# Performance work log

Measured on AMD Instinct MI355X. Metric: run time of the kernel, lower is better.

The kernel has to match this reference:

```python
import jax, jax.numpy as jnp
import numpy as np
from jax.scipy.special import logsumexp

BN_EPS = 1e-5
K_CLUSTERS = 32


def _conv1x1(x, W, b):
    # x: [B, Cin, N], W: [Cout, Cin] -> [B, Cout, N]
    return jnp.einsum('oc,bcn->bon', W, x) + b[None, :, None]


def _bn3(x, g, b):
    # BatchNorm1d (training mode, batch stats) over [B, C, N]
    m = x.mean(axis=(0, 2), keepdims=True)
    v = x.var(axis=(0, 2), keepdims=True)
    return g[None, :, None] * (x - m) / jnp.sqrt(v + BN_EPS) + b[None, :, None]


def _bn2(x, g, b):
    # BatchNorm1d (training mode, batch stats) over [B, C]
    m = x.mean(axis=0)
    v = x.var(axis=0)
    return g * (x - m) / jnp.sqrt(v + BN_EPS) + b


def _conv_proj(x, w1, b1, g1, t1, w2, b2, g2, t2, w3, b3):
    h = jax.nn.relu(_bn3(_conv1x1(x, w1, b1), g1, t1))
    h = jax.nn.relu(_bn3(_conv1x1(h, w2, b2), g2, t2))
    return _conv1x1(h, w3, b3)


def _mlp_proj(x, w1, b1, g1, t1, w2, b2, g2, t2, w3, b3):
    h = jax.nn.relu(_bn2(x @ w1.T + b1, g1, t1))
    h = jax.nn.relu(_bn2(h @ w2.T + b2, g2, t2))
    return h @ w3.T + b3


def _normalize(x, axis):
    n = jnp.linalg.norm(x, axis=axis, keepdims=True)
    return x / jnp.maximum(n, 1e-12)


def _sinkhorn_gamma(cost, p, q, eps=1e-3, thresh=1e-3, max_iter=25):
    # log-domain Sinkhorn with early stopping, mirrors the torch loop exactly
    logp = jnp.log(p + 1e-8)
    logq = jnp.log(q + 1e-8)

    def Kf(u, v):
        return (-cost + u[..., :, None] + v[..., None, :]) / eps

    def body(st):
        i, u, v, _ = st
        u0, v0 = u, v
        u = eps * (logp - logsumexp(Kf(u, v), axis=-1)) + u
        v = eps * (logq - logsumexp(Kf(u, v), axis=-2)) + v
        d = jnp.mean(jnp.sum(jnp.abs(u - u0), -1) + jnp.sum(jnp.abs(v - v0), -1))
        return i + 1, u, v, d

    def cond(st):
        return (st[0] < max_iter) & (st[3] >= thresh)

    init = (0, jnp.zeros_like(p), jnp.zeros_like(q), jnp.asarray(jnp.inf, cost.dtype))
    _, u, v, _ = jax.lax.while_loop(cond, body, init)
    return jnp.exp(Kf(u, v))


def _forward(features,
             cw1, cb1, cg1, ct1, cw2, cb2, cg2, ct2, cw3, cb3,
             pw1, pb1, pg1, pt1, pw2, pb2, pg2, pt2, pw3, pb3,
             mw1, mb1, mg1, mt1, mw2, mb2, mg2, mt2, mw3, mb3):
    bs, dim, num = features.shape
    Kc = K_CLUSTERS

    log_score = _conv_proj(features, cw1, cb1, cg1, ct1, cw2, cb2, cg2, ct2, cw3, cb3)  # [B,K,N]
    score = jax.nn.softmax(log_score, axis=1)
    pi = jax.lax.stop_gradient(jnp.clip(score.sum(-1), 1e-4)[:, None, :])  # [B,1,K]
    vlad = jnp.einsum('bkn,bdn->bdk', score, features) / pi  # [B,D,K] (mu == vlad)

    # no-grad Sinkhorn assignment (xyz is None branch, dst='fe')
    nf = _normalize(jax.lax.stop_gradient(features), axis=1)
    nmu = _normalize(jax.lax.stop_gradient(vlad), axis=1)
    cost = jax.lax.stop_gradient(2.0 - 2.0 * jnp.einsum('bdn,bdm->bnm', nf, nmu))  # [B,N,K]
    p = jnp.full((bs, num), 1.0 / num, dtype=features.dtype)
    q = jnp.full((bs, Kc), 1.0 / Kc, dtype=features.dtype)
    gamma = _sinkhorn_gamma(cost, p, q, eps=1e-3, thresh=1e-3, max_iter=25)
    assign = jax.lax.stop_gradient(num * jnp.swapaxes(gamma, -1, -2))  # [B,K,N]

    loss = -jnp.mean(jnp.sum(assign * jax.nn.log_softmax(log_score, axis=1), axis=1))

    c_vlad = _mlp_proj(jnp.max(vlad, axis=-1),
                       mw1, mb1, mg1, mt1, mw2, mb2, mg2, mt2, mw3, mb3)  # [B,proj]
    vlad_out = _conv_proj(vlad, pw1, pb1, pg1, pt1, pw2, pb2, pg2, pt2, pw3, pb3)  # [B,proj,K]
    return loss, vlad_out, c_vlad


def setup_inputs() -> dict:
    B, D, N, Kc, H, P = 8, 1024, 4096, 32, 512, 128
    key = jax.random.key(0)
    ks = jax.random.split(key, 16)

    def w(k, out_c, in_c):
        return (jax.random.normal(k, (out_c, in_c), jnp.float32) / np.sqrt(in_c)).astype(jnp.float32)

    d = {'features': jax.random.normal(ks[0], (B, D, N), jnp.float32)}
    # score conv head: D -> H -> H -> Kc  (hidden = dim // 2 = 512)
    d.update(cw1=w(ks[1], H, D), cb1=jnp.zeros(H), cg1=jnp.ones(H), ct1=jnp.zeros(H),
             cw2=w(ks[2], H, H), cb2=jnp.zeros(H), cg2=jnp.ones(H), ct2=jnp.zeros(H),
             cw3=w(ks[3], Kc, H), cb3=jnp.zeros(Kc))
    # projector conv: D -> 512 -> 512 -> P
    d.update(pw1=w(ks[4], H, D), pb1=jnp.zeros(H), pg1=jnp.ones(H), pt1=jnp.zeros(H),
             pw2=w(ks[5], H, H), pb2=jnp.zeros(H), pg2=jnp.ones(H), pt2=jnp.zeros(H),
             pw3=w(ks[6], P, H), pb3=jnp.zeros(P))
    # predictor MLP: D -> 512 -> 512 -> P
    d.update(mw1=w(ks[7], H, D), mb1=jnp.zeros(H), mg1=jnp.ones(H), mt1=jnp.zeros(H),
             mw2=w(ks[8], H, H), mb2=jnp.zeros(H), mg2=jnp.ones(H), mt2=jnp.zeros(H),
             mw3=w(ks[9], P, H), mb3=jnp.zeros(P))
    return d


def reference(features,
              cw1, cb1, cg1, ct1, cw2, cb2, cg2, ct2, cw3, cb3,
              pw1, pb1, pg1, pt1, pw2, pb2, pg2, pt2, pw3, pb3,
              mw1, mb1, mg1, mt1, mw2, mb2, mg2, mt2, mw3, mb3):
    return _forward(features,
                    cw1, cb1, cg1, ct1, cw2, cb2, cg2, ct2, cw3, cb3,
                    pw1, pb1, pg1, pt1, pw2, pb2, pg2, pt2, pw3, pb3,
                    mw1, mb1, mg1, mt1, mw2, mb2, mg2, mt2, mw3, mb3)
```

## Files before the change

### kernel.cpp

```cpp
#include <hip/hip_runtime.h>
#include <cmath>

#define BB 8
#define DD 1024
#define NP 4096
#define KC 32
#define HH 512
#define PP 128
#define NJB 16
#define BN_EPS 1e-5f

typedef unsigned short u16;
typedef unsigned long long u64;
typedef short s16x8 __attribute__((ext_vector_type(8)));
typedef float f32x4 __attribute__((ext_vector_type(4)));

__device__ __forceinline__ float waveReduceSum(float v) {
#pragma unroll
  for (int o = 32; o > 0; o >>= 1) v += __shfl_down(v, o, 64);
  return v;
}

__device__ __forceinline__ void split3(float y, short& h, short& m, short& l) {
  unsigned uy = __float_as_uint(y);
  h = (short)(uy >> 16);
  float r1 = y - __uint_as_float(uy & 0xFFFF0000u);
  unsigned um = __float_as_uint(r1);
  m = (short)(um >> 16);
  float r2 = r1 - __uint_as_float(um & 0xFFFF0000u);
  l = (short)(__float_as_uint(r2) >> 16);
}

__global__ __launch_bounds__(256) void convW3_all(
    const float* __restrict__ W1, u16* __restrict__ h1, u16* __restrict__ m1, u16* __restrict__ l1,
    const float* __restrict__ W2, u16* __restrict__ h2, u16* __restrict__ m2, u16* __restrict__ l2,
    const float* __restrict__ W3, u16* __restrict__ h3, u16* __restrict__ m3, u16* __restrict__ l3) {
  int z = blockIdx.z;
  const float* W; u16 *hb, *mb, *lb; int K, BM, MTt, KCH;
  if (z == 0)      { W = W1; hb = h1; mb = m1; lb = l1; K = 1024; BM = 128; MTt = 4; KCH = 32; }
  else if (z == 1) { W = W2; hb = h2; mb = m2; lb = l2; K = 512;  BM = 128; MTt = 4; KCH = 16; }
  else             { W = W3; hb = h3; mb = m3; lb = l3; K = 512;  BM = 32;  MTt = 1; KCH = 16; }
  int mt = blockIdx.x, kc = blockIdx.y;
  if (mt >= MTt || kc >= KCH) return;
  const int AU = BM * 4;
  for (int u = threadIdx.x; u < AU; u += 256) {
    int q = u / BM, m = u % BM;
    const float* wp = W + (size_t)(mt * BM + m) * K + kc * 32 + q * 8;
    s16x8 hv, mv, lv;
#pragma unroll
    for (int j = 0; j < 8; j++) {
      short h, mm, l; split3(wp[j], h, mm, l);
      hv[j] = h; mv[j] = mm; lv[j] = l;
    }
    size_t ob = ((size_t)(mt * KCH + kc)) * (size_t)(BM * 32) + (size_t)u * 8;
    *(s16x8*)(hb + ob) = hv;
    *(s16x8*)(mb + ob) = mv;
    *(s16x8*)(lb + ob) = lv;
  }
}

template<int BM, int MBLK, int MT, int NT, int WM, bool BNRELU>
__global__ __launch_bounds__(256) void gemm_mfma3(
    const u16* __restrict__ wh, const u16* __restrict__ wmid, const u16* __restrict__ wl,
    const float* __restrict__ bias, const float* __restrict__ X,
    const float* __restrict__ bnsc, const float* __restrict__ bnsh,
    float* __restrict__ Y, int K, int M) {
  __shared__ s16x8 AhS[BM * 4], AmS[BM * 4], AlS[BM * 4];
  __shared__ s16x8 BhS[512], BmS[512], BlS[512];
  const int KCH = K / 32;
  const int tid = threadIdx.x;
  const int bz = blockIdx.z;
  int bid = blockIdx.x;
  int xs = bid & 7, rr = bid >> 3;
  int m_idx = rr % MBLK;
  int n_idx = xs + 8 * (rr / MBLK);

  const int w = tid >> 6, l = tid & 63, q = l >> 4, col = l & 15;
  const int wm = (WM == 1) ? 0 : (w >> 1);
  const int wn = (WM == 1) ? w : (w & 1);
  constexpr int NA = (BM * 4 + 255) / 256;

  f32x4 acc[MT][NT];
#pragma unroll
  for (int i = 0; i < MT; i++)
#pragma unroll
    for (int j = 0; j < NT; j++) { acc[i][j][0] = 0.f; acc[i][j][1] = 0.f; acc[i][j][2] = 0.f; acc[i][j][3] = 0.f; }

  const short* Ah = (const short*)AhS;
  const short* Am = (const short*)AmS;
  const short* Al = (const short*)AlS;
  const short* Bh = (const short*)BhS;
  const short* Bm = (const short*)BmS;
  const short* Bl = (const short*)BlS;

  const float* Xb = X + (size_t)bz * (size_t)K * NP + (size_t)n_idx * 128;
  const size_t abase = (size_t)m_idx * KCH * (size_t)(BM * 32);

  s16x8 rAh[NA], rAm[NA], rAl[NA];
  float rB[2][8];

  {
    const s16x8* awh = (const s16x8*)(wh + abase);
    const s16x8* awm = (const s16x8*)(wmid + abase);
    const s16x8* awl = (const s16x8*)(wl + abase);
#pragma unroll
    for (int t = 0; t < NA; t++) {
      int u = tid + t * 256;
      if (u < BM * 4) { rAh[t] = awh[u]; rAm[t] = awm[u]; rAl[t] = awl[u]; }
    }
#pragma unroll
    for (int t = 0; t < 2; t++) {
      int u = tid + t * 256;
      int qq = u >> 7, n = u & 127;
      const float* fp = Xb + (size_t)(qq * 8) * NP + n;
#pragma unroll
      for (int j = 0; j < 8; j++) {
        float y = fp[(size_t)j * NP];
        if (BNRELU) y = fmaxf(fmaf(y, bnsc[qq * 8 + j], bnsh[qq * 8 + j]), 0.f);
        rB[t][j] = y;
      }
    }
  }

  for (int kc = 0; kc < KCH; kc++) {
#pragma unroll
    for (int t = 0; t < NA; t++) {
      int u = tid + t * 256;
      if (u < BM * 4) { AhS[u] = rAh[t]; AmS[u] = rAm[t]; AlS[u] = rAl[t]; }
    }
#pragma unroll
    for (int t = 0; t < 2; t++) {
      int u = tid + t * 256;
      s16x8 hv, mv, lv;
#pragma unroll
      for (int j = 0; j < 8; j++) {
        short h, mm, ll; split3(rB[t][j], h, mm, ll);
        hv[j] = h; mv[j] = mm; lv[j] = ll;
      }
      BhS[u] = hv; BmS[u] = mv; BlS[u] = lv;
    }
    __syncthreads();

    if (kc + 1 < KCH) {
      size_t ab = abase + (size_t)(kc + 1) * (size_t)(BM * 32);
      const s16x8* awh = (const s16x8*)(wh + ab);
      const s16x8* awm = (const s16x8*)(wmid + ab);
      const s16x8* awl = (const s16x8*)(wl + ab);
#pragma unroll
      for (int t = 0; t < NA; t++) {
        int u = tid + t * 256;
        if (u < BM * 4) { rAh[t] = awh[u]; rAm[t] = awm[u]; rAl[t] = awl[u]; }
      }
      const int kp = (kc + 1) * 32;
#pragma unroll
      for (int t = 0; t < 2; t++) {
        int u = tid + t * 256;
        int qq = u >> 7, n = u & 127;
        const float* fp = Xb + (size_t)(kp + qq * 8) * NP + n;
#pragma unroll
        for (int j = 0; j < 8; j++) {
          float y = fp[(size_t)j * NP];
          if (BNRELU) y = fmaxf(fmaf(y, bnsc[kp + qq * 8 + j], bnsh[kp + qq * 8 + j]), 0.f);
          rB[t][j] = y;
        }
      }
    }

    s16x8 ah[MT], am[MT], al[MT];
#pragma unroll
    for (int i = 0; i < MT; i++) {
      int off = (q * BM + wm * (MT * 16) + i * 16 + col) * 8;
      ah[i] = *(const s16x8*)(Ah + off);
      am[i] = *(const s16x8*)(Am + off);
      al[i] = *(const s16x8*)(Al + off);
    }
    __builtin_amdgcn_s_setprio(1);
#pragma unroll
    for (int j = 0; j < NT; j++) {
      int offb = (q * 128 + wn * (NT * 16) + j * 16 + col) * 8;
      s16x8 bh = *(const s16x8*)(Bh + offb);
      s16x8 bm = *(const s16x8*)(Bm + offb);
      s16x8 bl = *(const s16x8*)(Bl + offb);
#pragma unroll
      for (int i = 0; i < MT; i++) {
        acc[i][j] = __builtin_amdgcn_mfma_f32_16x16x32_bf16(ah[i], bh, acc[i][j], 0, 0, 0);
        acc[i][j] = __builtin_amdgcn_mfma_f32_16x16x32_bf16(ah[i], bm, acc[i][j], 0, 0, 0);
        acc[i][j] = __builtin_amdgcn_mfma_f32_16x16x32_bf16(am[i], bh, acc[i][j], 0, 0, 0);
        acc[i][j] = __builtin_amdgcn_mfma_f32_16x16x32_bf16(ah[i], bl, acc[i][j], 0, 0, 0);
        acc[i][j] = __builtin_amdgcn_mfma_f32_16x16x32_bf16(am[i], bm, acc[i][j], 0, 0, 0);
        acc[i][j] = __builtin_amdgcn_mfma_f32_16x16x32_bf16(al[i], bh, acc[i][j], 0, 0, 0);
      }
    }
    __builtin_amdgcn_s_setprio(0);
    __syncthreads();
  }
#pragma unroll
  for (int i = 0; i < MT; i++) {
#pragma unroll
    for (int r = 0; r < 4; r++) {
      int m = m_idx * BM + wm * (MT * 16) + i * 16 + q * 4 + r;
      float bv = bias[m];
#pragma unroll
      for (int j = 0; j < NT; j++) {
        int n = n_idx * 128 + wn * (NT * 16) + j * 16 + col;
        Y[((size_t)bz * M + m) * 4096 + n] = acc[i][j][r] + bv;
      }
    }
  }
}

__global__ __launch_bounds__(256) void bnstats(
    const float* __restrict__ Y, const float* __restrict__ g, const float* __restrict__ beta,
    float* __restrict__ scale, float* __restrict__ shift, int C, int N) {
  int c = blockIdx.x;
  float s = 0.f, sq = 0.f;
  for (int b = 0; b < BB; b++) {
    const float* p = Y + ((size_t)b * C + c) * N;
    for (int n = threadIdx.x; n < N; n += 256) { float v = p[n]; s += v; sq += v * v; }
  }
  __shared__ float shs[4], shq[4];
  int lane = threadIdx.x & 63, wid = threadIdx.x >> 6;
  s = waveReduceSum(s); sq = waveReduceSum(sq);
  if (lane == 0) { shs[wid] = s; shq[wid] = sq; }
  __syncthreads();
  if (threadIdx.x == 0) {
    float S = shs[0] + shs[1] + shs[2] + shs[3];
    float Q = shq[0] + shq[1] + shq[2] + shq[3];
    float cnt = (float)(BB * N);
    float mean = S / cnt;
    float var = Q / cnt - mean * mean;
    float sc = g[c] / sqrtf(var + BN_EPS);
    scale[c] = sc; shift[c] = beta[c] - mean * sc;
  }
}

__global__ __launch_bounds__(256) void softmax_pi(
    const float* __restrict__ LSm, float* __restrict__ score,
    float* __restrict__ lseArr, float* __restrict__ pi_raw) {
  int gidx = blockIdx.x * 256 + threadIdx.x;
  int b = gidx / NP, n = gidx % NP;
  const float* p = LSm + (size_t)b * KC * NP + n;
  float v[KC];
  float m = -1e30f;
#pragma unroll
  for (int k = 0; k < KC; k++) { v[k] = p[(size_t)k * NP]; m = fmaxf(m, v[k]); }
  float s = 0.f;
#pragma unroll
  for (int k = 0; k < KC; k++) { v[k] = expf(v[k] - m); s += v[k]; }
  float inv = 1.f / s;
  float* qq = score + (size_t)b * KC * NP + n;
#pragma unroll
  for (int k = 0; k < KC; k++) { v[k] *= inv; qq[(size_t)k * NP] = v[k]; }
  lseArr[gidx] = m + logf(s);
  __shared__ float ps[KC];
  if (threadIdx.x < KC) ps[threadIdx.x] = 0.f;
  __syncthreads();
  int lane = threadIdx.x & 63;
#pragma unroll
  for (int k = 0; k < KC; k++) {
    float w = waveReduceSum(v[k]);
    if (lane == 0) atomicAdd(&ps[k], w);
  }
  __syncthreads();
  if (threadIdx.x < KC) atomicAdd(&pi_raw[b * KC + threadIdx.x], ps[threadIdx.x]);
}

__global__ __launch_bounds__(256) void vlad_accum(
    const float* __restrict__ feat, const float* __restrict__ score, float* __restrict__ vlad) {
  const int SPLIT_LEN = NP / 8;
  int sp = blockIdx.x, dt = blockIdx.y, b = blockIdx.z;
  int d0 = dt * 128;
  int n_start = sp * SPLIT_LEN;
  __shared__ float As[32][132];
  __shared__ float Bs[32][36];
  int tid = threadIdx.x;
  int tx = tid % 16;
  int ty = tid / 16;
  float acc[8][2] = {};
  const float* fb = feat + (size_t)b * DD * NP;
  const float* sb = score + (size_t)b * KC * NP;
  for (int nc = 0; nc < SPLIT_LEN; nc += 32) {
    int n0 = n_start + nc;
    for (int i = tid; i < 128 * 32; i += 256) {
      int r = i >> 5, c = i & 31;
      As[c][r] = fb[(size_t)(d0 + r) * NP + n0 + c];
    }
    for (int i = tid; i < 32 * 32; i += 256) {
      int r = i >> 5, c = i & 31;
      Bs[c][r] = sb[(size_t)r * NP + n0 + c];
    }
    __syncthreads();
#pragma unroll 4
    for (int kk = 0; kk < 32; kk++) {
      float ra[8], rb[2];
#pragma unroll
      for (int i = 0; i < 8; i++) ra[i] = As[kk][ty * 8 + i];
      rb[0] = Bs[kk][tx * 2]; rb[1] = Bs[kk][tx * 2 + 1];
#pragma unroll
      for (int i = 0; i < 8; i++) { acc[i][0] = fmaf(ra[i], rb[0], acc[i][0]); acc[i][1] = fmaf(ra[i], rb[1], acc[i][1]); }
    }
    __syncthreads();
  }
#pragma unroll
  for (int i = 0; i < 8; i++)
#pragma unroll
    for (int j = 0; j < 2; j++)
      atomicAdd(&vlad[((size_t)b * DD + d0 + ty * 8 + i) * KC + tx * 2 + j], acc[i][j]);
}

__global__ __launch_bounds__(256) void vlad_fin(
    float* __restrict__ vlad, const float* __restrict__ pi_raw, float* __restrict__ gmax,
    float* __restrict__ nmusq) {
  int idx = blockIdx.x * 256 + threadIdx.x;
  int b = idx / DD;
  float* p = vlad + (size_t)idx * KC;
  const float* pr = pi_raw + b * KC;
  float gm = -1e30f;
  __shared__ float wk[4][KC];
  int lane = threadIdx.x & 63, wid = threadIdx.x >> 6;
#pragma unroll
  for (int k = 0; k < KC; k++) {
    float v = p[k] / fmaxf(pr[k], 1e-4f);
    p[k] = v;
    gm = fmaxf(gm, v);
    float s2 = waveReduceSum(v * v);
    if (lane == 0) wk[wid][k] = s2;
  }
  gmax[idx] = gm;
  __syncthreads();
  if (threadIdx.x < KC) {
    float t = wk[0][threadIdx.x] + wk[1][threadIdx.x] + wk[2][threadIdx.x] + wk[3][threadIdx.x];
    atomicAdd(&nmusq[b * KC + threadIdx.x], t);
  }
}

__global__ __launch_bounds__(256) void cost_accum(
    const float* __restrict__ feat, const float* __restrict__ vlad, float* __restrict__ costd,
    float* __restrict__ nfsq) {
  int sp = blockIdx.x, nt = blockIdx.y, b = blockIdx.z;
  int n0 = nt * 128;
  int d_start = sp * (DD / 4);
  __shared__ float As[32][132];
  __shared__ float Bs[32][36];
  __shared__ float nfs[128];
  int tid = threadIdx.x;
  int tx = tid % 16;
  int ty = tid / 16;
  float acc[8][2] = {};
  float sq = 0.f;
  const float* fb = feat + (size_t)b * DD * NP;
  const float* vb = vlad + (size_t)b * DD * KC;
  for (int dc = 0; dc < DD / 4; dc += 32) {
    int dd0 = d_start + dc;
    for (int i = tid; i < 32 * 128; i += 256) {
      int r = i >> 7, c = i & 127;
      float v = fb[(size_t)(dd0 + r) * NP + n0 + c];
      As[r][c] = v;
      sq = fmaf(v, v, sq);
    }
    for (int i = tid; i < 32 * 32; i += 256) {
      int r = i >> 5, c = i & 31;
      Bs[r][c] = vb[(size_t)(dd0 + r) * KC + c];
    }
    __syncthreads();
#pragma unroll 4
    for (int kk = 0; kk < 32; kk++) {
      float ra[8], rb[2];
#pragma unroll
      for (int i = 0; i < 8; i++) ra[i] = As[kk][ty * 8 + i];
      rb[0] = Bs[kk][tx * 2]; rb[1] = Bs[kk][tx * 2 + 1];
#pragma unroll
      for (int i = 0; i < 8; i++) { acc[i][0] = fmaf(ra[i], rb[0], acc[i][0]); acc[i][1] = fmaf(ra[i], rb[1], acc[i][1]); }
    }
    __syncthreads();
  }
#pragma unroll
  for (int i = 0; i < 8; i++)
#pragma unroll
    for (int j = 0; j < 2; j++)
      atomicAdd(&costd[((size_t)b * NP + n0 + ty * 8 + i) * KC + tx * 2 + j], acc[i][j]);
  if (tid < 128) nfs[tid] = 0.f;
  __syncthreads();
  atomicAdd(&nfs[tid & 127], sq);
  __syncthreads();
  if (tid < 128) atomicAdd(&nfsq[(size_t)b * NP + n0 + tid], nfs[tid]);
}

__global__ __launch_bounds__(256) void sinkhorn_all(
    const float* __restrict__ costd, const float* __restrict__ nfsq,
    const float* __restrict__ nmusq, u64* __restrict__ G,
    const float* __restrict__ LSm, const float* __restrict__ lseArr,
    float* __restrict__ out0, unsigned* __restrict__ flags,
    float logp, float logq) {
  const float EPS = 1e-3f, IEPS = 1000.f;
  int b = blockIdx.x / NJB, j = blockIdx.x % NJB;
  int tid = threadIdx.x;
  int n = j * 256 + tid;
  __shared__ float vsh[KC];
  __shared__ float nmS[KC];
  __shared__ float vals[256][33];
  __shared__ float red[KC][9];
  __shared__ float bmS[KC];
  __shared__ float redL[4];

  if (tid < KC) nmS[tid] = fmaxf(sqrtf(nmusq[b * KC + tid]), 1e-12f);
  __syncthreads();

  float c[KC];
  {
    const float* dp = costd + ((size_t)b * NP + n) * KC;
    float nf = fmaxf(sqrtf(nfsq[(size_t)b * NP + n]), 1e-12f);
#pragma unroll
    for (int k = 0; k < KC; k++) c[k] = 2.f - 2.f * dp[k] / (nf * nmS[k]);
  }

  const int kk = tid & 31, seg = tid >> 5;
  const int r0 = seg * 32;
  float u = 0.f;

  for (int t = 1; t <= 25; t++) {
    if (t > 1) {
      if (tid < NJB) {
        const unsigned* fp = flags + ((size_t)(t - 2) * BB + b) * NJB;
        while (__hip_atomic_load(&fp[tid], __ATOMIC_RELAXED, __HIP_MEMORY_SCOPE_AGENT) == 0u)
          __builtin_amdgcn_s_sleep(1);
      }
      __syncthreads();
    }
    if (tid < KC) {
      float v = 0.f;
      if (t > 1) {
        const u64* Gp = G + (((size_t)(t - 2) * BB + b) * NJB) * KC;
        float gm[NJB], gs[NJB];
#pragma unroll
        for (int jj = 0; jj < NJB; jj++) {
          u64 raw = __hip_atomic_load(&Gp[jj * KC + tid], __ATOMIC_RELAXED, __HIP_MEMORY_SCOPE_AGENT);
          gm[jj] = __uint_as_float((unsigned)raw);
          gs[jj] = __uint_as_float((unsigned)(raw >> 32));
// ... 46 lines not shown
      __hip_atomic_store(Gp, raw, __ATOMIC_RELAXED, __HIP_MEMORY_SCOPE_AGENT);
    }
    __syncthreads();
    if (tid == 0) {
      unsigned* fl = flags + ((size_t)(t - 1) * BB + b) * NJB + j;
      __hip_atomic_store(fl, 1u, __ATOMIC_RELAXED, __HIP_MEMORY_SCOPE_AGENT);
    }
  }

  if (tid < NJB) {
    const unsigned* fp = flags + ((size_t)24 * BB + b) * NJB;
    while (__hip_atomic_load(&fp[tid], __ATOMIC_RELAXED, __HIP_MEMORY_SCOPE_AGENT) == 0u)
      __builtin_amdgcn_s_sleep(1);
  }
  __syncthreads();
  __shared__ float v25S[KC];
  if (tid < KC) {
    const u64* Gp = G + (((size_t)24 * BB + b) * NJB) * KC;
    float gm[NJB], gs[NJB];
#pragma unroll
    for (int jj = 0; jj < NJB; jj++) {
      u64 raw = __hip_atomic_load(&Gp[jj * KC + tid], __ATOMIC_RELAXED, __HIP_MEMORY_SCOPE_AGENT);
      gm[jj] = __uint_as_float((unsigned)raw);
      gs[jj] = __uint_as_float((unsigned)(raw >> 32));
    }
    float m = -1e30f;
#pragma unroll
    for (int jj = 0; jj < NJB; jj++) m = fmaxf(m, gm[jj]);
    float s = 0.f;
#pragma unroll
    for (int jj = 0; jj < NJB; jj++) s += gs[jj] * expf(gm[jj] - m);
    v25S[tid] = EPS * logq - EPS * (m + logf(s));
  }
  __syncthreads();
  float lsev = lseArr[(size_t)b * NP + n];
  float part = 0.f;
#pragma unroll
  for (int k = 0; k < KC; k++) {
    float gamma = expf((u + v25S[k] - c[k]) * IEPS);
    float logsm = LSm[((size_t)b * KC + k) * NP + n] - lsev;
    part += gamma * logsm;
  }
  part *= (float)NP;
  int lane = tid & 63, wid = tid >> 6;
  part = waveReduceSum(part);
  if (lane == 0) redL[wid] = part;
  __syncthreads();
  if (tid == 0) {
    float tt = redL[0] + redL[1] + redL[2] + redL[3];
    atomicAdd(out0, -tt / (float)(BB * NP));
  }
}

template<int BM, int BN, int BK, int TM, int TN, bool BNRELU>
__global__ __launch_bounds__(256) void gemm_conv(
    const float* __restrict__ W, const float* __restrict__ bias,
    const float* __restrict__ X, float* __restrict__ Y,
    const float* __restrict__ bnscale, const float* __restrict__ bnshift,
    int M, int K, int N) {
  __shared__ float As[BK][BM + 4];
  __shared__ float Xs[BK][BN + 4];
  const int b = blockIdx.z;
  const int m0 = blockIdx.y * BM;
  const int n0 = blockIdx.x * BN;
  const int tid = threadIdx.x;
  const int tx = tid % (BN / TN);
  const int ty = tid / (BN / TN);
  const float* Xb = X + (size_t)b * K * N;
  float acc[TM][TN];
#pragma unroll
  for (int i = 0; i < TM; i++)
#pragma unroll
    for (int j = 0; j < TN; j++) acc[i][j] = 0.f;

  for (int k0 = 0; k0 < K; k0 += BK) {
    for (int i = tid; i < BM * BK; i += 256) {
      int r = i / BK, c = i % BK;
      As[c][r] = W[(size_t)(m0 + r) * K + k0 + c];
    }
    for (int i = tid; i < BK * BN; i += 256) {
      int r = i / BN, c = i % BN;
      float x = Xb[(size_t)(k0 + r) * N + n0 + c];
      if (BNRELU) x = fmaxf(fmaf(x, bnscale[k0 + r], bnshift[k0 + r]), 0.f);
      Xs[r][c] = x;
    }
    __syncthreads();
#pragma unroll 4
    for (int kk = 0; kk < BK; kk++) {
      float ra[TM], rb[TN];
#pragma unroll
      for (int i = 0; i < TM; i++) ra[i] = As[kk][ty * TM + i];
#pragma unroll
      for (int j = 0; j < TN; j++) rb[j] = Xs[kk][tx * TN + j];
#pragma unroll
      for (int i = 0; i < TM; i++)
#pragma unroll
        for (int j = 0; j < TN; j++) acc[i][j] = fmaf(ra[i], rb[j], acc[i][j]);
    }
    __syncthreads();
  }
#pragma unroll
  for (int i = 0; i < TM; i++) {
    float bm = bias[m0 + ty * TM + i];
#pragma unroll
    for (int j = 0; j < TN; j++)
      Y[((size_t)b * M + m0 + ty * TM + i) * N + n0 + tx * TN + j] = acc[i][j] + bm;
  }
}

template<bool BNRELU>
__global__ __launch_bounds__(256) void mlp_gemm(
    const float* __restrict__ W, const float* __restrict__ bias,
    const float* __restrict__ in, float* __restrict__ out,
    const float* __restrict__ sc, const float* __restrict__ sh, int M, int K) {
  int gw = (blockIdx.x * 256 + threadIdx.x) >> 6;
  int lane = threadIdx.x & 63;
  int s = gw / M, jj = gw % M;
  const float4* ip = (const float4*)(in + (size_t)s * K);
  const float4* wp = (const float4*)(W + (size_t)jj * K);
  float acc = 0.f;
  for (int c4 = lane; c4 < (K >> 2); c4 += 64) {
    float4 x = ip[c4];
    float4 w = wp[c4];
    if (BNRELU) {
      int cb = c4 * 4;
      x.x = fmaxf(fmaf(x.x, sc[cb + 0], sh[cb + 0]), 0.f);
      x.y = fmaxf(fmaf(x.y, sc[cb + 1], sh[cb + 1]), 0.f);
      x.z = fmaxf(fmaf(x.z, sc[cb + 2], sh[cb + 2]), 0.f);
      x.w = fmaxf(fmaf(x.w, sc[cb + 3], sh[cb + 3]), 0.f);
    }
    acc += x.x * w.x + x.y * w.y + x.z * w.z + x.w * w.w;
  }
  acc = waveReduceSum(acc);
  if (lane == 0) out[gw] = acc + bias[jj];
}

__global__ __launch_bounds__(256) void mlp_bnstats(
    const float* __restrict__ mat, const float* __restrict__ g, const float* __restrict__ beta,
    float* __restrict__ scale, float* __restrict__ shift, int M) {
  int j = blockIdx.x * 256 + threadIdx.x;
  if (j >= M) return;
  float s = 0.f, sq = 0.f;
  for (int si = 0; si < BB; si++) { float v = mat[si * M + j]; s += v; sq += v * v; }
  float mean = s / (float)BB;
  float var = sq / (float)BB - mean * mean;
  float sc = g[j] / sqrtf(var + BN_EPS);
  scale[j] = sc; shift[j] = beta[j] - mean * sc;
}

extern "C" void kernel_launch(void* const* d_in, const int* in_sizes, int n_in,
                              void* d_out, int out_size, void* d_ws, size_t ws_size,
                              hipStream_t stream) {
  const float* feat = (const float*)d_in[0];
  const float* cw1 = (const float*)d_in[1];  const float* cb1 = (const float*)d_in[2];
  const float* cg1 = (const float*)d_in[3];  const float* ct1 = (const float*)d_in[4];
  const float* cw2 = (const float*)d_in[5];  const float* cb2 = (const float*)d_in[6];
  const float* cg2 = (const float*)d_in[7];  const float* ct2 = (const float*)d_in[8];
  const float* cw3 = (const float*)d_in[9];  const float* cb3 = (const float*)d_in[10];
  const float* pw1 = (const float*)d_in[11]; const float* pb1 = (const float*)d_in[12];
  const float* pg1 = (const float*)d_in[13]; const float* pt1 = (const float*)d_in[14];
  const float* pw2 = (const float*)d_in[15]; const float* pb2 = (const float*)d_in[16];
  const float* pg2 = (const float*)d_in[17]; const float* pt2 = (const float*)d_in[18];
  const float* pw3 = (const float*)d_in[19]; const float* pb3 = (const float*)d_in[20];
  const float* mw1 = (const float*)d_in[21]; const float* mb1 = (const float*)d_in[22];
  const float* mg1 = (const float*)d_in[23]; const float* mt1 = (const float*)d_in[24];
  const float* mw2 = (const float*)d_in[25]; const float* mb2 = (const float*)d_in[26];
  const float* mg2 = (const float*)d_in[27]; const float* mt2 = (const float*)d_in[28];
  const float* mw3 = (const float*)d_in[29]; const float* mb3 = (const float*)d_in[30];
  float* out = (float*)d_out;

  char* p = (char*)d_ws;
  size_t off = 0;
  auto alloc = [&](size_t bytes) { char* r = p + off; off = (off + bytes + 255) & ~(size_t)255; return r; };
  float* Y1 = (float*)alloc(67108864);
  float* Y2 = (float*)alloc(67108864);
  u16* W1H = (u16*)alloc(1048576); u16* W1M = (u16*)alloc(1048576); u16* W1L = (u16*)alloc(1048576);
  u16* W2H = (u16*)alloc(524288);  u16* W2M = (u16*)alloc(524288);  u16* W2L = (u16*)alloc(524288);
  u16* W3H = (u16*)alloc(32768);   u16* W3M = (u16*)alloc(32768);   u16* W3L = (u16*)alloc(32768);
  float* SC1  = (float*)alloc(2048); float* SH1 = (float*)alloc(2048);
  float* SC2  = (float*)alloc(2048); float* SH2 = (float*)alloc(2048);
  float* PSC1 = (float*)alloc(2048); float* PSH1 = (float*)alloc(2048);
  float* PSC2 = (float*)alloc(2048); float* PSH2 = (float*)alloc(2048);
  float* MSC1 = (float*)alloc(2048); float* MSH1 = (float*)alloc(2048);
  float* MSC2 = (float*)alloc(2048); float* MSH2 = (float*)alloc(2048);
  char* q = (char*)Y1;
  size_t qoff = 0;
  auto qalloc = [&](size_t bytes) { char* r = q + qoff; qoff = (qoff + bytes + 255) & ~(size_t)255; return r; };
  float* LSC  = (float*)qalloc(4194304);
  float* SCRB = (float*)qalloc(4194304);
  float* LSE  = (float*)qalloc(131072);
  u64*   GBUF = (u64*)qalloc(819200);
  float* GMAX = (float*)qalloc(32768);
  float* MH1  = (float*)qalloc(16384);
  float* MH2  = (float*)qalloc(16384);
  float* T1   = (float*)qalloc(524288);
  float* T2   = (float*)qalloc(524288);
  const size_t MS_BYTES = 1024 + 1048576 + 4194304 + 131072 + 1024 + 16384;
  char* MS = qalloc(MS_BYTES);
  float* PIRAW = (float*)MS;
  float* VLAD  = (float*)(MS + 1024);
  float* COSTD = (float*)(MS + 1024 + 1048576);
  float* NFSQ  = (float*)(MS + 1024 + 1048576 + 4194304);
  float* NMUSQ = (float*)(MS + 1024 + 1048576 + 4194304 + 131072);
  unsigned* FLG = (unsigned*)(MS + 1024 + 1048576 + 4194304 + 131072 + 1024);

  hipMemsetAsync(d_out, 0, sizeof(float), stream);

  float logp = logf(1.0f / NP + 1e-8f);
  float logq = logf(1.0f / KC + 1e-8f);
  dim3 blk(256);

  convW3_all<<<dim3(4, 32, 3), blk, 0, stream>>>(
      cw1, W1H, W1M, W1L, cw2, W2H, W2M, W2L, cw3, W3H, W3M, W3L);

  gemm_mfma3<128, 4, 4, 4, 2, false><<<dim3(128, 1, 8), blk, 0, stream>>>(
      W1H, W1M, W1L, cb1, feat, nullptr, nullptr, Y1, 1024, 512);
  bnstats<<<dim3(512), blk, 0, stream>>>(Y1, cg1, ct1, SC1, SH1, 512, NP);
  gemm_mfma3<128, 4, 4, 4, 2, true><<<dim3(128, 1, 8), blk, 0, stream>>>(
      W2H, W2M, W2L, cb2, Y1, SC1, SH1, Y2, 512, 512);
  bnstats<<<dim3(512), blk, 0, stream>>>(Y2, cg2, ct2, SC2, SH2, 512, NP);
  hipMemsetAsync(MS, 0, MS_BYTES, stream);
  gemm_mfma3<32, 1, 2, 2, 1, true><<<dim3(32, 1, 8), blk, 0, stream>>>(
      W3H, W3M, W3L, cb3, Y2, SC2, SH2, LSC, 512, 32);

  softmax_pi<<<dim3(BB * NP / 256), blk, 0, stream>>>(LSC, SCRB, LSE, PIRAW);

  vlad_accum<<<dim3(8, DD / 128, BB), blk, 0, stream>>>(feat, SCRB, VLAD);
  vlad_fin<<<dim3(BB * DD / 256), blk, 0, stream>>>(VLAD, PIRAW, GMAX, NMUSQ);

  cost_accum<<<dim3(4, NP / 128, BB), blk, 0, stream>>>(feat, VLAD, COSTD, NFSQ);

  sinkhorn_all<<<dim3(BB * NJB), blk, 0, stream>>>(
      COSTD, NFSQ, NMUSQ, GBUF, LSC, LSE, out, FLG, logp, logq);

  mlp_gemm<false><<<dim3(BB * HH / 4), blk, 0, stream>>>(mw1, mb1, GMAX, MH1, nullptr, nullptr, HH, DD);
  mlp_bnstats<<<dim3(2), blk, 0, stream>>>(MH1, mg1, mt1, MSC1, MSH1, HH);
  mlp_gemm<true><<<dim3(BB * HH / 4), blk, 0, stream>>>(mw2, mb2, MH1, MH2, MSC1, MSH1, HH, HH);
  mlp_bnstats<<<dim3(2), blk, 0, stream>>>(MH2, mg2, mt2, MSC2, MSH2, HH);
  mlp_gemm<true><<<dim3(BB * PP / 4), blk, 0, stream>>>(mw3, mb3, MH2, out + 1 + BB * PP * KC, MSC2, MSH2, PP, HH);

  gemm_conv<64, 32, 16, 4, 2, false><<<dim3(1, HH / 64, BB), blk, 0, stream>>>(pw1, pb1, VLAD, T1, nullptr, nullptr, HH, DD, KC);
  bnstats<<<dim3(512), blk, 0, stream>>>(T1, pg1, pt1, PSC1, PSH1, HH, KC);
  gemm_conv<64, 32, 16, 4, 2, true><<<dim3(1, HH / 64, BB), blk, 0, stream>>>(pw2, pb2, T1, T2, PSC1, PSH1, HH, HH, KC);
  bnstats<<<dim3(512), blk, 0, stream>>>(T2, pg2, pt2, PSC2, PSH2, HH, KC);
  gemm_conv<64, 32, 16, 4, 2, true><<<dim3(1, PP / 64, BB), blk, 0, stream>>>(pw3, pb3, T2, out + 1, PSC2, PSH2, PP, HH, KC);
}
```

Measured before the change: 1.222 ms.

## Fuse BN stats, softmax and VLAD normalization into GEMM epilogues

Removes the separate bnstats, mlp_bnstats, softmax_pi and vlad_fin kernels. Each GEMM epilogue now accumulates per-channel sum and sum-of-squares via shared and global atomics, and consumers derive BN scale and shift in shared memory. The small conv3 GEMM computes the softmax, log-sum-exp and pi accumulation directly from its accumulators. The VLAD division by pi, gmax and norms move into cost_accum and the projector GEMM. This cuts extra full passes over the 8x512x4096 activations and several launches, at the cost of atomic contention and possible E[x^2]-mean^2 precision differences.

```diff
diff --git a/kernel.cpp b/kernel.cpp
--- a/kernel.cpp
+++ b/kernel.cpp
@@ -34,8 +34,14 @@
 __global__ __launch_bounds__(256) void convW3_all(
     const float* __restrict__ W1, u16* __restrict__ h1, u16* __restrict__ m1, u16* __restrict__ l1,
     const float* __restrict__ W2, u16* __restrict__ h2, u16* __restrict__ m2, u16* __restrict__ l2,
-    const float* __restrict__ W3, u16* __restrict__ h3, u16* __restrict__ m3, u16* __restrict__ l3) {
+    const float* __restrict__ W3, u16* __restrict__ h3, u16* __restrict__ m3, u16* __restrict__ l3,
+    float* __restrict__ zbuf) {
   int z = blockIdx.z;
+  if (z == 2 && blockIdx.x >= 1) {
+    int id = (blockIdx.x - 1) * 32 + blockIdx.y;
+    if (id < 24) zbuf[id * 256 + threadIdx.x] = 0.f;
+    return;
+  }
   const float* W; u16 *hb, *mb, *lb; int K, BM, MTt, KCH;
   if (z == 0)      { W = W1; hb = h1; mb = m1; lb = l1; K = 1024; BM = 128; MTt = 4; KCH = 32; }
   else if (z == 1) { W = W2; hb = h2; mb = m2; lb = l2; K = 512;  BM = 128; MTt = 4; KCH = 16; }
@@ -59,14 +65,18 @@
   }
 }
 
-template<int BM, int MBLK, int MT, int NT, int WM, bool BNRELU>
+template<int BM, int MBLK, int MT, int NT, int WM, bool BNRELU, bool ACCST, bool SMAX>
 __global__ __launch_bounds__(256) void gemm_mfma3(
     const u16* __restrict__ wh, const u16* __restrict__ wmid, const u16* __restrict__ wl,
     const float* __restrict__ bias, const float* __restrict__ X,
-    const float* __restrict__ bnsc, const float* __restrict__ bnsh,
-    float* __restrict__ Y, int K, int M) {
+    const float* __restrict__ insum, const float* __restrict__ insq,
+    const float* __restrict__ bng, const float* __restrict__ bnb, float cnt,
+    float* __restrict__ Y, int K, int M,
+    float* __restrict__ gsum, float* __restrict__ gsq,
+    float* __restrict__ score, float* __restrict__ lse, float* __restrict__ piraw) {
   __shared__ s16x8 AhS[BM * 4], AmS[BM * 4], AlS[BM * 4];
   __shared__ s16x8 BhS[512], BmS[512], BlS[512];
+  __shared__ float scS[512], shS[512];
   const int KCH = K / 32;
   const int tid = threadIdx.x;
   const int bz = blockIdx.z;
@@ -80,6 +90,16 @@
   const int wn = (WM == 1) ? w : (w & 1);
   constexpr int NA = (BM * 4 + 255) / 256;
 
+  if (BNRELU) {
+    for (int c0 = tid; c0 < K; c0 += 256) {
+      float mean = insum[c0] / cnt;
+      float var = insq[c0] / cnt - mean * mean;
+      float sc = bng[c0] / sqrtf(var + BN_EPS);
+      scS[c0] = sc; shS[c0] = bnb[c0] - mean * sc;
+    }
+    __syncthreads();
+  }
+
   f32x4 acc[MT][NT];
 #pragma unroll
   for (int i = 0; i < MT; i++)
@@ -116,7 +136,7 @@
 #pragma unroll
       for (int j = 0; j < 8; j++) {
         float y = fp[(size_t)j * NP];
-        if (BNRELU) y = fmaxf(fmaf(y, bnsc[qq * 8 + j], bnsh[qq * 8 + j]), 0.f);
+        if (BNRELU) y = fmaxf(fmaf(y, scS[qq * 8 + j], shS[qq * 8 + j]), 0.f);
         rB[t][j] = y;
       }
     }
@@ -160,7 +180,7 @@
 #pragma unroll
         for (int j = 0; j < 8; j++) {
           float y = fp[(size_t)j * NP];
-          if (BNRELU) y = fmaxf(fmaf(y, bnsc[kp + qq * 8 + j], bnsh[kp + qq * 8 + j]), 0.f);
+          if (BNRELU) y = fmaxf(fmaf(y, scS[kp + qq * 8 + j], shS[kp + qq * 8 + j]), 0.f);
           rB[t][j] = y;
         }
       }
@@ -194,75 +214,102 @@
     __builtin_amdgcn_s_setprio(0);
     __syncthreads();
   }
-#pragma unroll
-  for (int i = 0; i < MT; i++) {
-#pragma unroll
-    for (int r = 0; r < 4; r++) {
-      int m = m_idx * BM + wm * (MT * 16) + i * 16 + q * 4 + r;
-      float bv = bias[m];
-#pragma unroll
-      for (int j = 0; j < NT; j++) {
-        int n = n_idx * 128 + wn * (NT * 16) + j * 16 + col;
-        Y[((size_t)bz * M + m) * 4096 + n] = acc[i][j][r] + bv;
-      }
-    }
-  }
-}
-
-__global__ __launch_bounds__(256) void bnstats(
-    const float* __restrict__ Y, const float* __restrict__ g, const float* __restrict__ beta,
-    float* __restrict__ scale, float* __restrict__ shift, int C, int N) {
-  int c = blockIdx.x;
-  float s = 0.f, sq = 0.f;
-  for (int b = 0; b < BB; b++) {
-    const float* p = Y + ((size_t)b * C + c) * N;
-    for (int n = threadIdx.x; n < N; n += 256) { float v = p[n]; s += v; sq += v * v; }
-  }
-  __shared__ float shs[4], shq[4];
-  int lane = threadIdx.x & 63, wid = threadIdx.x >> 6;
-  s = waveReduceSum(s); sq = waveReduceSum(sq);
-  if (lane == 0) { shs[wid] = s; shq[wid] = sq; }
-  __syncthreads();
-  if (threadIdx.x == 0) {
-    float S = shs[0] + shs[1] + shs[2] + shs[3];
-    float Q = shq[0] + shq[1] + shq[2] + shq[3];
-    float cnt = (float)(BB * N);
-    float mean = S / cnt;
-    float var = Q / cnt - mean * mean;
-    float sc = g[c] / sqrtf(var + BN_EPS);
-    scale[c] = sc; shift[c] = beta[c] - mean * sc;
-  }
-}
-
-__global__ __launch_bounds__(256) void softmax_pi(
-    const float* __restrict__ LSm, float* __restrict__ score,
-    float* __restrict__ lseArr, float* __restrict__ pi_raw) {
-  int gidx = blockIdx.x * 256 + threadIdx.x;
-  int b = gidx / NP, n = gidx % NP;
-  const float* p = LSm + (size_t)b * KC * NP + n;
-  float v[KC];
-  float m = -1e30f;
-#pragma unroll
-  for (int k = 0; k < KC; k++) { v[k] = p[(size_t)k * NP]; m = fmaxf(m, v[k]); }
-  float s = 0.f;
-#pragma unroll
-  for (int k = 0; k < KC; k++) { v[k] = expf(v[k] - m); s += v[k]; }
-  float inv = 1.f / s;
-  float* qq = score + (size_t)b * KC * NP + n;
-#pragma unroll
-  for (int k = 0; k < KC; k++) { v[k] *= inv; qq[(size_t)k * NP] = v[k]; }
-  lseArr[gidx] = m + logf(s);
-  __shared__ float ps[KC];
-  if (threadIdx.x < KC) ps[threadIdx.x] = 0.f;
-  __syncthreads();
-  int lane = threadIdx.x & 63;
-#pragma unroll
-  for (int k = 0; k < KC; k++) {
-    float w = waveReduceSum(v[k]);
-    if (lane == 0) atomicAdd(&ps[k], w);
-  }
-  __syncthreads();
-  if (threadIdx.x < KC) atomicAdd(&pi_raw[b * KC + threadIdx.x], ps[threadIdx.x]);
+
+  if (!SMAX) {
+    float* red = (float*)AhS;
+    if (ACCST) {
+      if (tid < 2 * BM) red[tid] = 0.f;
+      __syncthreads();
+    }
+#pragma unroll
+    for (int i = 0; i < MT; i++) {
+#pragma unroll
+      for (int r = 0; r < 4; r++) {
+        int ml = wm * (MT * 16) + i * 16 + q * 4 + r;
+        int m = m_idx * BM + ml;
+        float bv = bias[m];
+        float ys = 0.f, yq = 0.f;
+#pragma unroll
+        for (int j = 0; j < NT; j++) {
+          int n = n_idx * 128 + wn * (NT * 16) + j * 16 + col;
+          float y = acc[i][j][r] + bv;
+          Y[((size_t)bz * M + m) * 4096 + n] = y;
+          ys += y; yq = fmaf(y, y, yq);
+        }
+        if (ACCST) {
+          atomicAdd(&red[ml * 2], ys);
+          atomicAdd(&red[ml * 2 + 1], yq);
+        }
+      }
+    }
+    if (ACCST) {
+      __syncthreads();
+      if (tid < BM) {
+        atomicAdd(&gsum[m_idx * BM + tid], red[tid * 2]);
+        atomicAdd(&gsq[m_idx * BM + tid], red[tid * 2 + 1]);
+      }
+    }
+  } else {
+    float yv[MT][NT][4];
+#pragma unroll
+    for (int i = 0; i < MT; i++) {
+#pragma unroll
+      for (int r = 0; r < 4; r++) {
+        int m = i * 16 + q * 4 + r;
+        float bv = bias[m];
+#pragma unroll
+        for (int j = 0; j < NT; j++) {
+          int n = n_idx * 128 + wn * (NT * 16) + j * 16 + col;
+          float y = acc[i][j][r] + bv;
+          Y[((size_t)bz * M + m) * 4096 + n] = y;
+          yv[i][j][r] = y;
+        }
+      }
+    }
+    float* redP = (float*)AhS;
+    if (tid < KC) redP[tid] = 0.f;
+    __syncthreads();
+    float pl[MT][4];
+#pragma unroll
+    for (int i = 0; i < MT; i++)
+#pragma unroll
+      for (int r = 0; r < 4; r++) pl[i][r] = 0.f;
+#pragma unroll
+    for (int j = 0; j < NT; j++) {
+      float mx = -1e30f;
+#pragma unroll
+      for (int i = 0; i < MT; i++)
+#pragma unroll
+        for (int r = 0; r < 4; r++) mx = fmaxf(mx, yv[i][j][r]);
+      mx = fmaxf(mx, __shfl_xor(mx, 16, 64));
+      mx = fmaxf(mx, __shfl_xor(mx, 32, 64));
+      float e[MT][4]; float s = 0.f;
+#pragma unroll
+      for (int i = 0; i < MT; i++)
+#pragma unroll
+        for (int r = 0; r < 4; r++) { e[i][r] = expf(yv[i][j][r] - mx); s += e[i][r]; }
+      s += __shfl_xor(s, 16, 64);
+      s += __shfl_xor(s, 32, 64);
+      float inv = 1.f / s;
+      int n = n_idx * 128 + wn * (NT * 16) + j * 16 + col;
+#pragma unroll
+      for (int i = 0; i < MT; i++)
+#pragma unroll
+        for (int r = 0; r < 4; r++) {
+          float sv = e[i][r] * inv;
+          int m = i * 16 + q * 4 + r;
+          score[((size_t)bz * KC + m) * NP + n] = sv;
+          pl[i][r] += sv;
+        }
+      if ((tid & 48) == 0) lse[(size_t)bz * NP + n] = mx + logf(s);
+    }
+#pragma unroll
+    for (int i = 0; i < MT; i++)
+#pragma unroll
+      for (int r = 0; r < 4; r++) atomicAdd(&redP[i * 16 + q * 4 + r], pl[i][r]);
+    __syncthreads();
+    if (tid < KC) atomicAdd(&piraw[bz * KC + tid], redP[tid]);
+  }
 }
 
 __global__ __launch_bounds__(256) void vlad_accum(
@@ -308,46 +355,25 @@
       atomicAdd(&vlad[((size_t)b * DD + d0 + ty * 8 + i) * KC + tx * 2 + j], acc[i][j]);
 }
 
-__global__ __launch_bounds__(256) void vlad_fin(
-    float* __restrict__ vlad, const float* __restrict__ pi_raw, float* __restrict__ gmax,
-    float* __restrict__ nmusq) {
-  int idx = blockIdx.x * 256 + threadIdx.x;
-  int b = idx / DD;
-  float* p = vlad + (size_t)idx * KC;
-  const float* pr = pi_raw + b * KC;
-  float gm = -1e30f;
-  __shared__ float wk[4][KC];
-  int lane = threadIdx.x & 63, wid = threadIdx.x >> 6;
-#pragma unroll
-  for (int k = 0; k < KC; k++) {
-    float v = p[k] / fmaxf(pr[k], 1e-4f);
-    p[k] = v;
-    gm = fmaxf(gm, v);
-    float s2 = waveReduceSum(v * v);
-    if (lane == 0) wk[wid][k] = s2;
-  }
-  gmax[idx] = gm;
-  __syncthreads();
-  if (threadIdx.x < KC) {
-    float t = wk[0][threadIdx.x] + wk[1][threadIdx.x] + wk[2][threadIdx.x] + wk[3][threadIdx.x];
-    atomicAdd(&nmusq[b * KC + threadIdx.x], t);
-  }
-}
-
 __global__ __launch_bounds__(256) void cost_accum(
-    const float* __restrict__ feat, const float* __restrict__ vlad, float* __restrict__ costd,
-    float* __restrict__ nfsq) {
+    const float* __restrict__ feat, const float* __restrict__ vlad,
+    const float* __restrict__ piraw, float* __restrict__ costd,
+    float* __restrict__ nfsq, float* __restrict__ nmusq, float* __restrict__ gmax) {
   int sp = blockIdx.x, nt = blockIdx.y, b = blockIdx.z;
   int n0 = nt * 128;
   int d_start = sp * (DD / 4);
   __shared__ float As[32][132];
   __shared__ float Bs[32][36];
   __shared__ float nfs[128];
+  __shared__ float piS[KC];
+  __shared__ float nms[KC];
   int tid = threadIdx.x;
   int tx = tid % 16;
   int ty = tid / 16;
+  if (tid < KC) { piS[tid] = fmaxf(piraw[b * KC + tid], 1e-4f); nms[tid] = 0.f; }
+  __syncthreads();
   float acc[8][2] = {};
-  float sq = 0.f;
+  float sq = 0.f, nm_local = 0.f;
   const float* fb = feat + (size_t)b * DD * NP;
   const float* vb = vlad + (size_t)b * DD * KC;
   for (int dc = 0; dc < DD / 4; dc += 32) {
@@ -360,9 +386,17 @@
     }
     for (int i = tid; i < 32 * 32; i += 256) {
       int r = i >> 5, c = i & 31;
-      Bs[r][c] = vb[(size_t)(dd0 + r) * KC + c];
-    }
-    __syncthreads();
+      float v = vb[(size_t)(dd0 + r) * KC + c] / piS[c];
+      Bs[r][c] = v;
+      if (nt == 0) nm_local = fmaf(v, v, nm_local);
+    }
+    __syncthreads();
+    if (nt == 0 && tid < 32) {
+      float gm = -1e30f;
+#pragma unroll
+      for (int c = 0; c < KC; c++) gm = fmaxf(gm, Bs[tid][c]);
+      gmax[(size_t)b * DD + dd0 + tid] = gm;
+    }
 #pragma unroll 4
     for (int kk = 0; kk < 32; kk++) {
       float ra[8], rb[2];
@@ -382,8 +416,10 @@
   if (tid < 128) nfs[tid] = 0.f;
   __syncthreads();
   atomicAdd(&nfs[tid & 127], sq);
+  if (nt == 0) atomicAdd(&nms[tid & 31], nm_local);
   __syncthreads();
   if (tid < 128) atomicAdd(&nfsq[(size_t)b * NP + n0 + tid], nfs[tid]);
+  if (nt == 0 && tid < KC) atomicAdd(&nmusq[b * KC + tid], nms[tid]);
 }
 
 __global__ __launch_bounds__(256) void sinkhorn_all(
@@ -536,20 +572,37 @@
   }
 }
 
-template<int BM, int BN, int BK, int TM, int TN, bool BNRELU>
+template<int BM, int BN, int BK, int TM, int TN, bool BNRELU, bool ACCST, bool PDIV>
 __global__ __launch_bounds__(256) void gemm_conv(
     const float* __restrict__ W, const float* __restrict__ bias,
     const float* __restrict__ X, float* __restrict__ Y,
-    const float* __restrict__ bnscale, const float* __restrict__ bnshift,
+    const float* __restrict__ pidiv,
+    const float* __restrict__ insum, const float* __restrict__ insq,
+    const float* __restrict__ bng, const float* __restrict__ bnb, float cnt,
+    float* __restrict__ gsum, float* __restrict__ gsq,
     int M, int K, int N) {
   __shared__ float As[BK][BM + 4];
   __shared__ float Xs[BK][BN + 4];
+  __shared__ float scS[512], shS[512];
+  __shared__ float piS[BN + 4];
   const int b = blockIdx.z;
   const int m0 = blockIdx.y * BM;
   const int n0 = blockIdx.x * BN;
   const int tid = threadIdx.x;
   const int tx = tid % (BN / TN);
   const int ty = tid / (BN / TN);
+  if (PDIV) {
+    if (tid < N) piS[tid] = fmaxf(pidiv[b * N + tid], 1e-4f);
+  }
+  if (BNRELU) {
+    for (int c0 = tid; c0 < K; c0 += 256) {
+      float mean = insum[c0] / cnt;
+      float var = insq[c0] / cnt - mean * mean;
+      float sc = bng[c0] / sqrtf(var + BN_EPS);
+      scS[c0] = sc; shS[c0] = bnb[c0] - mean * sc;
+    }
+  }
+  if (PDIV || BNRELU) __syncthreads();
   const float* Xb = X + (size_t)b * K * N;
   float acc[TM][TN];
 #pragma unroll
@@ -565,7 +618,8 @@
     for (int i = tid; i < BK * BN; i += 256) {
       int r = i / BN, c = i % BN;
       float x = Xb[(size_t)(k0 + r) * N + n0 + c];
-      if (BNRELU) x = fmaxf(fmaf(x, bnscale[k0 + r], bnshift[k0 + r]), 0.f);
+      if (PDIV) x /= piS[n0 + c];
+      if (BNRELU) x = fmaxf(fmaf(x, scS[k0 + r], shS[k0 + r]), 0.f);
       Xs[r][c] = x;
     }
     __syncthreads();
@@ -583,22 +637,56 @@
     }
     __syncthreads();
   }
+  float* red = (float*)As;
+  if (ACCST) {
+    if (tid < 2 * BM) red[tid] = 0.f;
+    __syncthreads();
+  }
 #pragma unroll
   for (int i = 0; i < TM; i++) {
-    float bm = bias[m0 + ty * TM + i];
-#pragma unroll
-    for (int j = 0; j < TN; j++)
-      Y[((size_t)b * M + m0 + ty * TM + i) * N + n0 + tx * TN + j] = acc[i][j] + bm;
-  }
-}
-
-template<bool BNRELU>
+    int ml = ty * TM + i;
+    float bm = bias[m0 + ml];
+    float ys = 0.f, yq = 0.f;
+#pragma unroll
+    for (int j = 0; j < TN; j++) {
+      float y = acc[i][j] + bm;
+      Y[((size_t)b * M + m0 + ml) * N + n0 + tx * TN + j] = y;
+      ys += y; yq = fmaf(y, y, yq);
+    }
+    if (ACCST) {
+      atomicAdd(&red[ml * 2], ys);
+      atomicAdd(&red[ml * 2 + 1], yq);
+    }
+  }
+  if (ACCST) {
+    __syncthreads();
+    if (tid < BM) {
+      atomicAdd(&gsum[m0 + tid], red[tid * 2]);
+      atomicAdd(&gsq[m0 + tid], red[tid * 2 + 1]);
+    }
+  }
+}
+
+template<bool BNRELU, bool ACCST>
 __global__ __launch_bounds__(256) void mlp_gemm(
     const float* __restrict__ W, const float* __restrict__ bias,
     const float* __restrict__ in, float* __restrict__ out,
-    const float* __restrict__ sc, const float* __restrict__ sh, int M, int K) {
-  int gw = (blockIdx.x * 256 + threadIdx.x) >> 6;
-  int lane = threadIdx.x & 63;
+    const float* __restrict__ insum, const float* __restrict__ insq,
+    const float* __restrict__ g, const float* __restrict__ beta,
+    float* __restrict__ gsum, float* __restrict__ gsq, int M, int K) {
+  __shared__ float scS[512], shS[512];
+  int tid = threadIdx.x;
+  if (BNRELU) {
+    for (int c0 = tid; c0 < K; c0 += 256) {
+      float mean = insum[c0] * 0.125f;
+      float var = insq[c0] * 0.125f - mean * mean;
+      float sc = g[c0] / sqrtf(var + BN_EPS);
+      scS[c0] = sc; shS[c0] = beta[c0] - mean * sc;
+    }
+    __syncthreads();
+  }
+  int gw = (blockIdx.x * 256 + tid) >> 6;
+  int lane = tid & 63;
   int s = gw / M, jj = gw % M;
   const float4* ip = (const float4*)(in + (size_t)s * K);
   const float4* wp = (const float4*)(W + (size_t)jj * K);
@@ -608,28 +696,19 @@
     float4 w = wp[c4];
     if (BNRELU) {
       int cb = c4 * 4;
-      x.x = fmaxf(fmaf(x.x, sc[cb + 0], sh[cb + 0]), 0.f);
-      x.y = fmaxf(fmaf(x.y, sc[cb + 1], sh[cb + 1]), 0.f);
-      x.z = fmaxf(fmaf(x.z, sc[cb + 2], sh[cb + 2]), 0.f);
-      x.w = fmaxf(fmaf(x.w, sc[cb + 3], sh[cb + 3]), 0.f);
+      x.x = fmaxf(fmaf(x.x, scS[cb + 0], shS[cb + 0]), 0.f);
+      x.y = fmaxf(fmaf(x.y, scS[cb + 1], shS[cb + 1]), 0.f);
+      x.z = fmaxf(fmaf(x.z, scS[cb + 2], shS[cb + 2]), 0.f);
+      x.w = fmaxf(fmaf(x.w, scS[cb + 3], shS[cb + 3]), 0.f);
     }
     acc += x.x * w.x + x.y * w.y + x.z * w.z + x.w * w.w;
   }
   acc = waveReduceSum(acc);
-  if (lane == 0) out[gw] = acc + bias[jj];
-}
-
-__global__ __launch_bounds__(256) void mlp_bnstats(
-    const float* __restrict__ mat, const float* __restrict__ g, const float* __restrict__ beta,
-    float* __restrict__ scale, float* __restrict__ shift, int M) {
-  int j = blockIdx.x * 256 + threadIdx.x;
-  if (j >= M) return;
-  float s = 0.f, sq = 0.f;
-  for (int si = 0; si < BB; si++) { float v = mat[si * M + j]; s += v; sq += v * v; }
-  float mean = s / (float)BB;
-  float var = sq / (float)BB - mean * mean;
-  float sc = g[j] / sqrtf(var + BN_EPS);
-  scale[j] = sc; shift[j] = beta[j] - mean * sc;
+  if (lane == 0) {
+    float y = acc + bias[jj];
+    out[gw] = y;
+    if (ACCST) { atomicAdd(&gsum[jj], y); atomicAdd(&gsq[jj], y * y); }
+  }
 }
 
 extern "C" void kernel_launch(void* const* d_in, const int* in_sizes, int n_in,
@@ -661,12 +740,13 @@
   u16* W1H = (u16*)alloc(1048576); u16* W1M = (u16*)alloc(1048576); u16* W1L = (u16*)alloc(1048576);
   u16* W2H = (u16*)alloc(524288);  u16* W2M = (u16*)alloc(524288);  u16* W2L = (u16*)alloc(524288);
   u16* W3H = (u16*)alloc(32768);   u16* W3M = (u16*)alloc(32768);   u16* W3L = (u16*)alloc(32768);
-  float* SC1  = (float*)alloc(2048); float* SH1 = (float*)alloc(2048);
-  float* SC2  = (float*)alloc(2048); float* SH2 = (float*)alloc(2048);
-  float* PSC1 = (float*)alloc(2048); float* PSH1 = (float*)alloc(2048);
-  float* PSC2 = (float*)alloc(2048); float* PSH2 = (float*)alloc(2048);
-  float* MSC1 = (float*)alloc(2048); float* MSH1 = (float*)alloc(2048);
-  float* MSC2 = (float*)alloc(2048); float* MSH2 = (float*)alloc(2048);
+  float* BNACC = (float*)alloc(24576);
+  float* GS1 = BNACC + 0,    * GQ1 = BNACC + 512;
+  float* GS2 = BNACC + 1024, * GQ2 = BNACC + 1536;
+  float* MSS1 = BNACC + 2048, * MSQ1 = BNACC + 2560;
+  float* MSS2 = BNACC + 3072, * MSQ2 = BNACC + 3584;
+  float* PS1 = BNACC + 4096, * PQ1 = BNACC + 4608;
+  float* PS2 = BNACC + 5120, * PQ2 = BNACC + 5632;
   char* q = (char*)Y1;
   size_t qoff = 0;
   auto qalloc = [&](size_t bytes) { char* r = q + qoff; qoff = (qoff + bytes + 255) & ~(size_t)255; return r; };
@@ -692,40 +772,43 @@
 
   float logp = logf(1.0f / NP + 1e-8f);
   float logq = logf(1.0f / KC + 1e-8f);
+  const float CNT_BN = (float)(BB * NP);
+  const float CNT_PJ = (float)(BB * KC);
   dim3 blk(256);
 
   convW3_all<<<dim3(4, 32, 3), blk, 0, stream>>>(
-      cw1, W1H, W1M, W1L, cw2, W2H, W2M, W2L, cw3, W3H, W3M, W3L);
-
-  gemm_mfma3<128, 4, 4, 4, 2, false><<<dim3(128, 1, 8), blk, 0, stream>>>(
-      W1H, W1M, W1L, cb1, feat, nullptr, nullptr, Y1, 1024, 512);
-  bnstats<<<dim3(512), blk, 0, stream>>>(Y1, cg1, ct1, SC1, SH1, 512, NP);
-  gemm_mfma3<128, 4, 4, 4, 2, true><<<dim3(128, 1, 8), blk, 0, stream>>>(
-      W2H, W2M, W2L, cb2, Y1, SC1, SH1, Y2, 512, 512);
-  bnstats<<<dim3(512), blk, 0, stream>>>(Y2, cg2, ct2, SC2, SH2, 512, NP);
+      cw1, W1H, W1M, W1L, cw2, W2H, W2M, W2L, cw3, W3H, W3M, W3L, BNACC);
+
+  gemm_mfma3<128, 4, 4, 4, 2, false, true, false><<<dim3(128, 1, 8), blk, 0, stream>>>(
+      W1H, W1M, W1L, cb1, feat, nullptr, nullptr, nullptr, nullptr, 0.f,
+      Y1, 1024, 512, GS1, GQ1, nullptr, nullptr, nullptr);
+  gemm_mfma3<128, 4, 4, 4, 2, true, true, false><<<dim3(128, 1, 8), blk, 0, stream>>>(
+      W2H, W2M, W2L, cb2, Y1, GS1, GQ1, cg1, ct1, CNT_BN,
+      Y2, 512, 512, GS2, GQ2, nullptr, nullptr, nullptr);
   hipMemsetAsync(MS, 0, MS_BYTES, stream);
-  gemm_mfma3<32, 1, 2, 2, 1, true><<<dim3(32, 1, 8), blk, 0, stream>>>(
-      W3H, W3M, W3L, cb3, Y2, SC2, SH2, LSC, 512, 32);
-
-  softmax_pi<<<dim3(BB * NP / 256), blk, 0, stream>>>(LSC, SCRB, LSE, PIRAW);
+  gemm_mfma3<32, 1, 2, 2, 1, true, false, true><<<dim3(32, 1, 8), blk, 0, stream>>>(
+      W3H, W3M, W3L, cb3, Y2, GS2, GQ2, cg2, ct2, CNT_BN,
+      LSC, 512, 32, nullptr, nullptr, SCRB, LSE, PIRAW);
 
   vlad_accum<<<dim3(8, DD / 128, BB), blk, 0, stream>>>(feat, SCRB, VLAD);
-  vlad_fin<<<dim3(BB * DD / 256), blk, 0, stream>>>(VLAD, PIRAW, GMAX, NMUSQ);
-
-  cost_accum<<<dim3(4, NP / 128, BB), blk, 0, stream>>>(feat, VLAD, COSTD, NFSQ);
+
+  cost_accum<<<dim3(4, NP / 128, BB), blk, 0, stream>>>(
+      feat, VLAD, PIRAW, COSTD, NFSQ, NMUSQ, GMAX);
 
   sinkhorn_all<<<dim3(BB * NJB), blk, 0, stream>>>(
       COSTD, NFSQ, NMUSQ, GBUF, LSC, LSE, out, FLG, logp, logq);
 
-  mlp_gemm<false><<<dim3(BB * HH / 4), blk, 0, stream>>>(mw1, mb1, GMAX, MH1, nullptr, nullptr, HH, DD);
-  mlp_bnstats<<<dim3(2), blk, 0, stream>>>(MH1, mg1, mt1, MSC1, MSH1, HH);
-  mlp_gemm<true><<<dim3(BB * HH / 4), blk, 0, stream>>>(mw2, mb2, MH1, MH2, MSC1, MSH1, HH, HH);
-  mlp_bnstats<<<dim3(2), blk, 0, stream>>>(MH2, mg2, mt2, MSC2, MSH2, HH);
-  mlp_gemm<true><<<dim3(BB * PP / 4), blk, 0, stream>>>(mw3, mb3, MH2, out + 1 + BB * PP * KC, MSC2, MSH2, PP, HH);
-
-  gemm_conv<64, 32, 16, 4, 2, false><<<dim3(1, HH / 64, BB), blk, 0, stream>>>(pw1, pb1, VLAD, T1, nullptr, nullptr, HH, DD, KC);
-  bnstats<<<dim3(512), blk, 0, stream>>>(T1, pg1, pt1, PSC1, PSH1, HH, KC);
-  gemm_conv<64, 32, 16, 4, 2, true><<<dim3(1, HH / 64, BB), blk, 0, stream>>>(pw2, pb2, T1, T2, PSC1, PSH1, HH, HH, KC);
-  bnstats<<<dim3(512), blk, 0, stream>>>(T2, pg2, pt2, PSC2, PSH2, HH, KC);
-  gemm_conv<64, 32, 16, 4, 2, true><<<dim3(1, PP / 64, BB), blk, 0, stream>>>(pw3, pb3, T2, out + 1, PSC2, PSH2, PP, HH, KC);
-}
+  mlp_gemm<false, true><<<dim3(BB * HH / 4), blk, 0, stream>>>(
+      mw1, mb1, GMAX, MH1, nullptr, nullptr, nullptr, nullptr, MSS1, MSQ1, HH, DD);
+  mlp_gemm<true, true><<<dim3(BB * HH / 4), blk, 0, stream>>>(
+      mw2, mb2, MH1, MH2, MSS1, MSQ1, mg1, mt1, MSS2, MSQ2, HH, HH);
+  mlp_gemm<true, false><<<dim3(BB * PP / 4), blk, 0, stream>>>(
+      mw3, mb3, MH2, out + 1 + BB * PP * KC, MSS2, MSQ2, mg2, mt2, nullptr, nullptr, PP, HH);
+
+  gemm_conv<64, 32, 16, 4, 2, false, true, true><<<dim3(1, HH / 64, BB), blk, 0, stream>>>(
+      pw1, pb1, VLAD, T1, PIRAW, nullptr, nullptr, nullptr, nullptr, 0.f, PS1, PQ1, HH, DD, KC);
+  gemm_conv<64, 32, 16, 4, 2, true, true, false><<<dim3(1, HH / 64, BB), blk, 0, stream>>>(
+      pw2, pb2, T1, T2, nullptr, PS1, PQ1, pg1, pt1, CNT_PJ, PS2, PQ2, HH, HH, KC);
+  gemm_conv<64, 32, 16, 4, 2, true, false, false><<<dim3(1, PP / 64, BB), blk, 0, stream>>>(
+      pw3, pb3, T2, out + 1, nullptr, PS2, PQ2, pg2, pt2, CNT_PJ, nullptr, nullptr, PP, HH, KC);
+}
```

New measurement: 1.226 ms. About the same (+0.3%).
